# Kernel optimization log

Hardware: AMD Instinct MI355X
Metric: run time of the kernel (lower is better)

## Reference

```python
import jax, jax.numpy as jnp
import numpy as np

N, E = 50000, 800000
IN_F, HID, NCLS, NLAYERS = 64, 64, 2, 3
BN_EPS = 1e-5


def batch_norm(x, gamma, beta):
    # training-mode BatchNorm1d: biased batch statistics over the node/edge dim
    m = jnp.mean(x, axis=0)
    v = jnp.var(x, axis=0)
    return gamma * (x - m) * jax.lax.rsqrt(v + BN_EPS) + beta


def setup_inputs() -> dict:
    key = jax.random.key(0)
    ks = jax.random.split(key, 24)
    L, Lp1 = NLAYERS, NLAYERS + 1

    def lin(k, fan_in, shape):
        bound = 1.0 / np.sqrt(fan_in)
        return jax.random.uniform(k, shape, jnp.float32, -bound, bound)

    return {
        "h": jax.random.normal(ks[0], (N, IN_F), jnp.float32),
        "src": jax.random.randint(ks[1], (E,), 0, N, jnp.int32),
        "dst": jax.random.randint(ks[2], (E,), 0, N, jnp.int32),
        "emb_W": lin(ks[3], IN_F, (IN_F, HID)),
        "emb_b": lin(ks[4], IN_F, (HID,)),
        "mlp_W1": lin(ks[5], HID, (L, HID, HID)),
        "mlp_b1": lin(ks[6], HID, (L, HID)),
        "mlp_bn_g": jnp.ones((L, HID), jnp.float32),
        "mlp_bn_b": jnp.zeros((L, HID), jnp.float32),
        "mlp_W2": lin(ks[7], HID, (L, HID, HID)),
        "mlp_b2": lin(ks[8], HID, (L, HID)),
        "apply_bn_g": jnp.ones((L, HID), jnp.float32),
        "apply_bn_b": jnp.zeros((L, HID), jnp.float32),
        "out_bn_g": jnp.ones((L, HID), jnp.float32),
        "out_bn_b": jnp.zeros((L, HID), jnp.float32),
        "pred_W1": lin(ks[9], 2 * HID, (Lp1, 2 * HID, HID)),
        "pred_b1": lin(ks[10], 2 * HID, (Lp1, HID)),
        "pred_W2": lin(ks[11], HID, (Lp1, HID, NCLS)),
        "pred_b2": lin(ks[12], HID, (Lp1, NCLS)),
    }


def reference(h, src, dst, emb_W, emb_b, mlp_W1, mlp_b1, mlp_bn_g, mlp_bn_b,
              mlp_W2, mlp_b2, apply_bn_g, apply_bn_b, out_bn_g, out_bn_b,
              pred_W1, pred_b1, pred_W2, pred_b2):
    n_layers = mlp_W1.shape[0]
    n_nodes = h.shape[0]

    def edge_feat(hn):
        # concat src and dst node features per edge -> [E, 2*HID]
        return jnp.concatenate([hn[src], hn[dst]], axis=1)

    hn = h @ emb_W + emb_b  # embedding_h
    edge_reps = [edge_feat(hn)]

    for i in range(n_layers):
        # GINConv (sum aggregation, eps=0): (1+eps)*h_v + sum_{u->v} h_u
        agg = jax.ops.segment_sum(hn[src], dst, num_segments=n_nodes)
        z = hn + agg
        # MLP (depth 2): Linear -> BN -> ReLU -> Linear
        z = jax.nn.relu(batch_norm(z @ mlp_W1[i] + mlp_b1[i], mlp_bn_g[i], mlp_bn_b[i]))
        z = z @ mlp_W2[i] + mlp_b2[i]
        # ApplyNodeFunc: BN + ReLU
        z = jax.nn.relu(batch_norm(z, apply_bn_g[i], apply_bn_b[i]))
        # outer per-layer BN + ReLU
        hn = jax.nn.relu(batch_norm(z, out_bn_g[i], out_bn_b[i]))
        edge_reps.append(edge_feat(hn))

    # sum of per-layer edge predictions: Linear(2h->h) -> ReLU -> Linear(h->ncls)
    score = jnp.zeros((src.shape[0], pred_W2.shape[-1]), h.dtype)
    for i, e in enumerate(edge_reps):
        score = score + jax.nn.relu(e @ pred_W1[i] + pred_b1[i]) @ pred_W2[i] + pred_b2[i]
    return score
```

## Files before the change

### kernel.cpp

```cpp
#include <hip/hip_runtime.h>
#include <hip/hip_bf16.h>


#define BN_EPS 1e-5f

static __device__ __forceinline__ float bf2f(ushort u) {
  return __uint_as_float(((unsigned)u) << 16);
}

__global__ __launch_bounds__(256) void hist_kernel(const int* __restrict__ dst,
                                                   int* __restrict__ deg, int E) {
  int i = blockIdx.x * blockDim.x + threadIdx.x;
  int stride = gridDim.x * blockDim.x;
  for (; i < E; i += stride) atomicAdd(&deg[dst[i]], 1);
}

__global__ __launch_bounds__(256) void scan1_kernel(const int* __restrict__ deg,
                                                    int* __restrict__ rowstart,
                                                    int* __restrict__ partials, int N) {
  __shared__ int wsum[4];
  int tid = threadIdx.x;
  int lane = tid & 63, w = tid >> 6;
  int base = blockIdx.x * 1024 + tid * 4;
  int d0 = 0, d1 = 0, d2 = 0, d3 = 0;
  if (base + 3 < N) {
    int4 v = *reinterpret_cast<const int4*>(deg + base);
    d0 = v.x; d1 = v.y; d2 = v.z; d3 = v.w;
  } else {
    if (base + 0 < N) d0 = deg[base + 0];
    if (base + 1 < N) d1 = deg[base + 1];
    if (base + 2 < N) d2 = deg[base + 2];
  }
  int t0 = d0, t1 = t0 + d1, t2 = t1 + d2, t3 = t2 + d3;
  int tot = t3;
  int inc = tot;
#pragma unroll
  for (int off = 1; off < 64; off <<= 1) {
    int v = __shfl_up(inc, off);
    if (lane >= off) inc += v;
  }
  if (lane == 63) wsum[w] = inc;
  __syncthreads();
  int woff = 0;
  for (int k = 0; k < w; ++k) woff += wsum[k];
  int excl = woff + inc - tot;
  if (base + 0 < N) rowstart[base + 0] = excl;
  if (base + 1 < N) rowstart[base + 1] = excl + t0;
  if (base + 2 < N) rowstart[base + 2] = excl + t1;
  if (base + 3 < N) rowstart[base + 3] = excl + t2;
  if (tid == 255) partials[blockIdx.x] = excl + t3;
}

__global__ __launch_bounds__(64) void scan2_kernel(int* __restrict__ partials,
                                                   int* __restrict__ rowstart_end,
                                                   int NB) {
  int lane = threadIdx.x;
  int v = (lane < NB) ? partials[lane] : 0;
  int inc = v;
#pragma unroll
  for (int off = 1; off < 64; off <<= 1) {
    int t = __shfl_up(inc, off);
    if (lane >= off) inc += t;
  }
  if (lane < NB) partials[lane] = inc - v;
  if (lane == 63) *rowstart_end = inc;
}

__global__ __launch_bounds__(256) void scan3_kernel(const int* __restrict__ partials,
                                                    int* __restrict__ rowstart,
                                                    int* __restrict__ cursor, int N) {
  int off = partials[blockIdx.x];
  int base = blockIdx.x * 1024 + threadIdx.x * 4;
#pragma unroll
  for (int k = 0; k < 4; ++k) {
    int i = base + k;
    if (i < N) {
      int r = rowstart[i] + off;
      rowstart[i] = r;
      cursor[i] = r;
    }
  }
}

__global__ __launch_bounds__(256) void fill_kernel(const int* __restrict__ src,
                                                   const int* __restrict__ dst,
                                                   int* __restrict__ cursor,
                                                   int* __restrict__ eidx,
                                                   int* __restrict__ eord, int E) {
  int i = blockIdx.x * blockDim.x + threadIdx.x;
  int stride = gridDim.x * blockDim.x;
  for (; i < E; i += stride) {
    int p = atomicAdd(&cursor[dst[i]], 1);
    eidx[p] = src[i];
    eord[p] = i;
  }
}

template <int TR>
__global__ __launch_bounds__(256) void agg_kernel(
    const float* __restrict__ c, const ushort* __restrict__ cb,
    const int* __restrict__ rowstart, const int* __restrict__ eidx,
    const float* __restrict__ stats_in, const float* __restrict__ g_in,
    const float* __restrict__ b_in, float* __restrict__ z, int N) {
  int lane = threadIdx.x & 63;
  int v = blockIdx.x * 4 + (threadIdx.x >> 6);
  if (v >= N) return;
  float sc = 1.f, sh = 0.f;
  if (TR) {
    float invN = 1.0f / (float)N;
    float m = stats_in[lane] * invN;
    float var = stats_in[64 + lane] * invN - m * m;
    sc = g_in[lane] * rsqrtf(var + BN_EPS);
    sh = b_in[lane] - m * sc;
  }
  float x0 = c[(size_t)v * 64 + lane];
  float acc = TR ? fmaxf(x0 * sc + sh, 0.f) : x0;
  int p = rowstart[v], pe = rowstart[v + 1];
  for (; p + 8 <= pe; p += 8) {
    int u[8];
#pragma unroll
    for (int k = 0; k < 8; ++k) u[k] = eidx[p + k];
    float x[8];
#pragma unroll
    for (int k = 0; k < 8; ++k) x[k] = bf2f(cb[(size_t)u[k] * 64 + lane]);
#pragma unroll
    for (int k = 0; k < 8; ++k) acc += TR ? fmaxf(x[k] * sc + sh, 0.f) : x[k];
  }
  if (p + 4 <= pe) {
    int u[4];
#pragma unroll
    for (int k = 0; k < 4; ++k) u[k] = eidx[p + k];
#pragma unroll
    for (int k = 0; k < 4; ++k) {
      float x = bf2f(cb[(size_t)u[k] * 64 + lane]);
      acc += TR ? fmaxf(x * sc + sh, 0.f) : x;
    }
    p += 4;
  }
  for (; p < pe; ++p) {
    float x = bf2f(cb[(size_t)eidx[p] * 64 + lane]);
    acc += TR ? fmaxf(x * sc + sh, 0.f) : x;
  }
  z[(size_t)v * 64 + lane] = acc;
}

__global__ __launch_bounds__(256) void gemm64_kernel(
    const float* __restrict__ in, const float* __restrict__ W,
    const float* __restrict__ bias, const float* __restrict__ stats_in,
    const float* __restrict__ g_in, const float* __restrict__ b_in,
    float* __restrict__ out, float* __restrict__ stats_out,
    __hip_bfloat16* __restrict__ out_bf, int N) {
  __shared__ float sW[64][64];
  __shared__ float sx[32][64];
  __shared__ float red[2][4][64];
  int tid = threadIdx.x;
  int lane = tid & 63, w = tid >> 6;
  int n0 = blockIdx.x * 32;
#pragma unroll
  for (int r = 0; r < 16; ++r) {
    int idx = r * 256 + tid;
    sW[idx >> 6][idx & 63] = W[idx];
  }
  float sc = 1.f, sh = 0.f;
  if (stats_in) {
    float invN = 1.0f / (float)N;
    float m = stats_in[lane] * invN;
    float var = stats_in[64 + lane] * invN - m * m;
    sc = g_in[lane] * rsqrtf(var + BN_EPS);
    sh = b_in[lane] - m * sc;
  }
#pragma unroll
  for (int r = 0; r < 8; ++r) {
    int idx = r * 256 + tid;
    int n = n0 + (idx >> 6);
    float x = (n < N) ? in[(size_t)n * 64 + lane] : 0.f;
    if (stats_in) x = fmaxf(x * sc + sh, 0.f);
    sx[idx >> 6][lane] = x;
  }
  __syncthreads();
  float acc[8];
  float bz = bias ? bias[lane] : 0.f;
#pragma unroll
  for (int j = 0; j < 8; ++j) acc[j] = bz;
  for (int k = 0; k < 64; ++k) {
    float wv = sW[k][lane];
#pragma unroll
    for (int j = 0; j < 8; ++j) acc[j] = fmaf(sx[w * 8 + j][k], wv, acc[j]);
  }
  float ps = 0.f, pq = 0.f;
#pragma unroll
  for (int j = 0; j < 8; ++j) {
    int n = n0 + w * 8 + j;
    if (n < N) {
      out[(size_t)n * 64 + lane] = acc[j];
      if (out_bf) out_bf[(size_t)n * 64 + lane] = __float2bfloat16(acc[j]);
      ps += acc[j];
      pq += acc[j] * acc[j];
    }
  }
  if (stats_out) {
    red[0][w][lane] = ps;
    red[1][w][lane] = pq;
    __syncthreads();
    if (w == 0) {
      float s = red[0][0][lane] + red[0][1][lane] + red[0][2][lane] + red[0][3][lane];
      float q = red[1][0][lane] + red[1][1][lane] + red[1][2][lane] + red[1][3][lane];
      atomicAdd(&stats_out[lane], s);
      atomicAdd(&stats_out[64 + lane], q);
    }
  }
}

__global__ __launch_bounds__(256) void proj_kernel(
    const float* __restrict__ c, const float* __restrict__ W1,
    const float* __restrict__ b1, const float* __restrict__ stats_in,
    const float* __restrict__ g_in, const float* __restrict__ b_in,
    __hip_bfloat16* __restrict__ P1, __hip_bfloat16* __restrict__ P2, int N) {
  __shared__ float sWa[64][64];
  __shared__ float sWb[64][64];
  __shared__ float sx[32][64];
  int tid = threadIdx.x, lane = tid & 63, w = tid >> 6;
  int n0 = blockIdx.x * 32;
#pragma unroll
  for (int r = 0; r < 16; ++r) {
    int idx = r * 256 + tid;
    sWa[idx >> 6][idx & 63] = W1[idx];
    sWb[idx >> 6][idx & 63] = W1[4096 + idx];
  }
  float sc = 1.f, sh = 0.f;
  if (stats_in) {
    float invN = 1.0f / (float)N;
    float m = stats_in[lane] * invN;
    float var = stats_in[64 + lane] * invN - m * m;
    sc = g_in[lane] * rsqrtf(var + BN_EPS);
    sh = b_in[lane] - m * sc;
  }
#pragma unroll
  for (int r = 0; r < 8; ++r) {
    int idx = r * 256 + tid;
    int n = n0 + (idx >> 6);
    float x = (n < N) ? c[(size_t)n * 64 + lane] : 0.f;
    if (stats_in) x = fmaxf(x * sc + sh, 0.f);
    sx[idx >> 6][lane] = x;
  }
  __syncthreads();
  float a1[8], a2[8];
  float bz = b1[lane];
#pragma unroll
  for (int j = 0; j < 8; ++j) { a1[j] = bz; a2[j] = 0.f; }
  for (int k = 0; k < 64; ++k) {
    float wa = sWa[k][lane];
    float wb = sWb[k][lane];
#pragma unroll
    for (int j = 0; j < 8; ++j) {
      float x = sx[w * 8 + j][k];
      a1[j] = fmaf(x, wa, a1[j]);
      a2[j] = fmaf(x, wb, a2[j]);
    }
  }
#pragma unroll
  for (int j = 0; j < 8; ++j) {
    int n = n0 + w * 8 + j;
    if (n < N) {
      P1[(size_t)n * 64 + lane] = __float2bfloat16(a1[j]);
      P2[(size_t)n * 64 + lane] = __float2bfloat16(a2[j]);
    }
  }
}

__global__ __launch_bounds__(256) void bnrelu_kernel(
    const float* __restrict__ in, const float* __restrict__ stats_in,
    const float* __restrict__ g_in, const float* __restrict__ b_in,
    float* __restrict__ out, float* __restrict__ stats_out,
    __hip_bfloat16* __restrict__ out_bf, int N) {
  __shared__ float red[2][4][64];
  int tid = threadIdx.x;
  int lane = tid & 63, w = tid >> 6;
  float invN = 1.0f / (float)N;
  float m = stats_in[lane] * invN;
  float var = stats_in[64 + lane] * invN - m * m;
  float sc = g_in[lane] * rsqrtf(var + BN_EPS);
  float sh = b_in[lane] - m * sc;
  float ps = 0.f, pq = 0.f;
  int rows_per_grid = gridDim.x * (blockDim.x >> 6);
  for (int n = blockIdx.x * (blockDim.x >> 6) + w; n < N; n += rows_per_grid) {
    float x = fmaxf(in[(size_t)n * 64 + lane] * sc + sh, 0.f);
    out[(size_t)n * 64 + lane] = x;
    if (out_bf) out_bf[(size_t)n * 64 + lane] = __float2bfloat16(x);
    ps += x;
    pq += x * x;
  }
  if (stats_out) {
    red[0][w][lane] = ps;
    red[1][w][lane] = pq;
    __syncthreads();
    if (w == 0) {
      float s = red[0][0][lane] + red[0][1][lane] + red[0][2][lane] + red[0][3][lane];
      float q = red[1][0][lane] + red[1][1][lane] + red[1][2][lane] + red[1][3][lane];
      atomicAdd(&stats_out[lane], s);
      atomicAdd(&stats_out[64 + lane], q);
    }
  }
}

__global__ __launch_bounds__(256) void edge_score_csr_kernel(
    const ushort* __restrict__ P1, const ushort* __restrict__ P2,
    const int* __restrict__ rowstart, const int* __restrict__ eidx,
    const int* __restrict__ eord, const float* __restrict__ W2,
    const float* __restrict__ b2, float* __restrict__ out, int N, int first) {
  int lane = threadIdx.x & 63;
  int v = blockIdx.x * 4 + (threadIdx.x >> 6);
  if (v >= N) return;
  int sub = lane & 7;
  int grp = lane >> 3;
  float w[16];
  const float4* wp = reinterpret_cast<const float4*>(W2 + sub * 16);
#pragma unroll
  for (int k = 0; k < 4; ++k) {
    float4 t = wp[k];
    w[4 * k + 0] = t.x; w[4 * k + 1] = t.y; w[4 * k + 2] = t.z; w[4 * k + 3] = t.w;
  }
  float bb0 = b2[0], bb1 = b2[1];
  uint4 pb = *reinterpret_cast<const uint4*>(P2 + (size_t)v * 64 + sub * 8);
  unsigned bv[4] = {pb.x, pb.y, pb.z, pb.w};
  int p0 = rowstart[v], p1 = rowstart[v + 1];
  for (int p = p0 + grp; p < p1; p += 8) {
    int s = eidx[p];
    int e = eord[p];
    uint4 pa = *reinterpret_cast<const uint4*>(P1 + (size_t)s * 64 + sub * 8);
    unsigned av[4] = {pa.x, pa.y, pa.z, pa.w};
    float q0 = 0.f, q1 = 0.f;
#pragma unroll
    for (int k = 0; k < 4; ++k) {
      float a_lo = __uint_as_float(av[k] << 16);
      float a_hi = __uint_as_float(av[k] & 0xffff0000u);
      float b_lo = __uint_as_float(bv[k] << 16);
      float b_hi = __uint_as_float(bv[k] & 0xffff0000u);
      float v0 = fmaxf(a_lo + b_lo, 0.f);
      float v1 = fmaxf(a_hi + b_hi, 0.f);
      q0 = fmaf(v0, w[4 * k + 0], fmaf(v1, w[4 * k + 2], q0));
      q1 = fmaf(v0, w[4 * k + 1], fmaf(v1, w[4 * k + 3], q1));
    }
#pragma unroll
    for (int mm = 1; mm < 8; mm <<= 1) {
      q0 += __shfl_xor(q0, mm);
      q1 += __shfl_xor(q1, mm);
    }
    if (sub == 0) {
      float o0 = q0 + bb0, o1 = q1 + bb1;
      if (!first) {
        o0 += out[(size_t)e * 2];
        o1 += out[(size_t)e * 2 + 1];
      }
      out[(size_t)e * 2] = o0;
      out[(size_t)e * 2 + 1] = o1;
    }
  }
}

extern "C" void kernel_launch(void* const* d_in, const int* in_sizes, int n_in,
                              void* d_out, int out_size, void* d_ws, size_t ws_size,
                              hipStream_t stream) {
  const float* h          = (const float*)d_in[0];
  const int*   src        = (const int*)d_in[1];
  const int*   dst        = (const int*)d_in[2];
  const float* emb_W      = (const float*)d_in[3];
  const float* emb_b      = (const float*)d_in[4];
  const float* mlp_W1     = (const float*)d_in[5];
  const float* mlp_b1     = (const float*)d_in[6];
  const float* mlp_bn_g   = (const float*)d_in[7];
  const float* mlp_bn_b   = (const float*)d_in[8];
  const float* mlp_W2     = (const float*)d_in[9];
  const float* mlp_b2     = (const float*)d_in[10];
  const float* apply_bn_g = (const float*)d_in[11];
  const float* apply_bn_b = (const float*)d_in[12];
  const float* out_bn_g   = (const float*)d_in[13];
  const float* out_bn_b   = (const float*)d_in[14];
  const float* pred_W1    = (const float*)d_in[15];
  const float* pred_b1    = (const float*)d_in[16];
  const float* pred_W2    = (const float*)d_in[17];
  const float* pred_b2    = (const float*)d_in[18];

  const int N = in_sizes[0] / 64;
  const int E = in_sizes[1];
  const size_t NF = (size_t)N * 64;
  const int NB1 = (N + 1023) / 1024;

  float* ws = (float*)d_ws;
  float* c  = ws;
  float* zb = c + NF;
  float* z1 = zb + NF;
  float* z2 = z1 + NF;
  __hip_bfloat16* cb = (__hip_bfloat16*)(z2 + NF);
  __hip_bfloat16* P1 = cb + NF;
  __hip_bfloat16* P2 = P1 + NF;
  int* eidx     = (int*)(P2 + NF);
  int* eord     = eidx + E;
  int* rowstart = eord + E;
  int* cursor   = rowstart + (N + 64);
  int* partials = cursor + (N + 64);
  int* deg      = partials + 64;
  float* stats  = (float*)(deg + (N + 64));

  size_t need = (size_t)((char*)(stats + 9 * 128) - (char*)d_ws);
  if (need > ws_size) return;

  hipMemsetAsync(deg, 0, ((size_t)(N + 64) + 9 * 128) * sizeof(int), stream);

  const int gemmBlocks = (N + 31) / 32;
  const int nodeBlocks = (N + 3) / 4;

  gemm64_kernel<<<gemmBlocks, 256, 0, stream>>>(h, emb_W, emb_b, nullptr, nullptr,
                                                nullptr, c, nullptr, cb, N);
  hist_kernel<<<1024, 256, 0, stream>>>(dst, deg, E);
  scan1_kernel<<<NB1, 256, 0, stream>>>(deg, rowstart, partials, N);
  scan2_kernel<<<1, 64, 0, stream>>>(partials, rowstart + N, NB1);
  scan3_kernel<<<NB1, 256, 0, stream>>>(partials, rowstart, cursor, N);
  fill_kernel<<<1024, 256, 0, stream>>>(src, dst, cursor, eidx, eord, E);

  proj_kernel<<<gemmBlocks, 256, 0, stream>>>(c, pred_W1, pred_b1, nullptr, nullptr,
                                              nullptr, P1, P2, N);
  edge_score_csr_kernel<<<nodeBlocks, 256, 0, stream>>>(
      (const ushort*)P1, (const ushort*)P2, rowstart, eidx, eord, pred_W2, pred_b2,
      (float*)d_out, N, 1);

  for (int i = 0; i < 3; ++i) {
    float* st1 = stats + (size_t)(3 * i + 0) * 128;
    float* st2 = stats + (size_t)(3 * i + 1) * 128;
    float* st3 = stats + (size_t)(3 * i + 2) * 128;
    const float* stP = (i == 0) ? nullptr : stats + (size_t)(3 * (i - 1) + 2) * 128;
    const float* gP  = (i == 0) ? nullptr : out_bn_g + (i - 1) * 64;
    const float* bP  = (i == 0) ? nullptr : out_bn_b + (i - 1) * 64;

    if (i == 0)
      agg_kernel<0><<<nodeBlocks, 256, 0, stream>>>(c, (const ushort*)cb, rowstart,
                                                    eidx, nullptr, nullptr, nullptr,
                                                    zb, N);
    else
      agg_kernel<1><<<nodeBlocks, 256, 0, stream>>>(c, (const ushort*)cb, rowstart,
                                                    eidx, stP, gP, bP, zb, N);
    gemm64_kernel<<<gemmBlocks, 256, 0, stream>>>(zb, mlp_W1 + (size_t)i * 4096,
                                                  mlp_b1 + i * 64, nullptr, nullptr,
                                                  nullptr, z1, st1, nullptr, N);
    gemm64_kernel<<<gemmBlocks, 256, 0, stream>>>(z1, mlp_W2 + (size_t)i * 4096,
                                                  mlp_b2 + i * 64, st1,
                                                  mlp_bn_g + i * 64, mlp_bn_b + i * 64,
                                                  z2, st2, nullptr, N);
    bnrelu_kernel<<<784, 256, 0, stream>>>(z2, st2, apply_bn_g + i * 64,
                                           apply_bn_b + i * 64, c, st3, cb, N);
    proj_kernel<<<gemmBlocks, 256, 0, stream>>>(c, pred_W1 + (size_t)(i + 1) * 8192,
                                                pred_b1 + (i + 1) * 64, st3,
                                                out_bn_g + i * 64, out_bn_b + i * 64,
                                                P1, P2, N);
    edge_score_csr_kernel<<<nodeBlocks, 256, 0, stream>>>(
        (const ushort*)P1, (const ushort*)P2, rowstart, eidx, eord,
        pred_W2 + (i + 1) * 128, pred_b2 + (i + 1) * 2, (float*)d_out, N, 0);
  }
}
```

Before: 928.1 us.

## Fuse aggregation into first MLP GEMM, pack CSR edges, accumulate scores in CSR order

Fuses the GIN neighbour aggregation with the first MLP linear layer, so the aggregated features go straight into shared memory instead of a round trip through a global buffer. Packs the CSR source index and original edge id into one int2 array. Edge scores now accumulate in CSR order, coalesced, in a scratch buffer, with a single scatter at the end replacing the random read-modify-write per layer. The second scan kernel is folded into the third. The trade-off is that each fused block now gathers 8 nodes per wave serially, which cuts parallelism in the gather phase, and the extra scatter pass adds traffic.

```diff
diff --git a/kernel.cpp b/kernel.cpp
--- a/kernel.cpp
+++ b/kernel.cpp
@@ -51,26 +51,25 @@
   if (tid == 255) partials[blockIdx.x] = excl + t3;
 }
 
-__global__ __launch_bounds__(64) void scan2_kernel(int* __restrict__ partials,
-                                                   int* __restrict__ rowstart_end,
-                                                   int NB) {
-  int lane = threadIdx.x;
-  int v = (lane < NB) ? partials[lane] : 0;
-  int inc = v;
-#pragma unroll
-  for (int off = 1; off < 64; off <<= 1) {
-    int t = __shfl_up(inc, off);
-    if (lane >= off) inc += t;
-  }
-  if (lane < NB) partials[lane] = inc - v;
-  if (lane == 63) *rowstart_end = inc;
-}
-
 __global__ __launch_bounds__(256) void scan3_kernel(const int* __restrict__ partials,
                                                     int* __restrict__ rowstart,
-                                                    int* __restrict__ cursor, int N) {
-  int off = partials[blockIdx.x];
-  int base = blockIdx.x * 1024 + threadIdx.x * 4;
+                                                    int* __restrict__ cursor,
+                                                    int N, int NB, int E) {
+  __shared__ int s_off;
+  int tid = threadIdx.x;
+  if (tid < 64) {
+    int v = (tid < NB) ? partials[tid] : 0;
+    int inc = v;
+#pragma unroll
+    for (int off = 1; off < 64; off <<= 1) {
+      int t = __shfl_up(inc, off);
+      if (tid >= off) inc += t;
+    }
+    if (tid == (int)blockIdx.x) s_off = inc - v;
+  }
+  __syncthreads();
+  int off = s_off;
+  int base = blockIdx.x * 1024 + tid * 4;
 #pragma unroll
   for (int k = 0; k < 4; ++k) {
     int i = base + k;
@@ -80,68 +79,102 @@
       cursor[i] = r;
     }
   }
+  if (blockIdx.x == 0 && tid == 0) rowstart[N] = E;
 }
 
 __global__ __launch_bounds__(256) void fill_kernel(const int* __restrict__ src,
                                                    const int* __restrict__ dst,
                                                    int* __restrict__ cursor,
-                                                   int* __restrict__ eidx,
-                                                   int* __restrict__ eord, int E) {
+                                                   int2* __restrict__ epack, int E) {
   int i = blockIdx.x * blockDim.x + threadIdx.x;
   int stride = gridDim.x * blockDim.x;
   for (; i < E; i += stride) {
     int p = atomicAdd(&cursor[dst[i]], 1);
-    eidx[p] = src[i];
-    eord[p] = i;
+    epack[p] = make_int2(src[i], i);
   }
 }
 
 template <int TR>
-__global__ __launch_bounds__(256) void agg_kernel(
+__global__ __launch_bounds__(256) void agg_gemm_kernel(
     const float* __restrict__ c, const ushort* __restrict__ cb,
-    const int* __restrict__ rowstart, const int* __restrict__ eidx,
-    const float* __restrict__ stats_in, const float* __restrict__ g_in,
-    const float* __restrict__ b_in, float* __restrict__ z, int N) {
-  int lane = threadIdx.x & 63;
-  int v = blockIdx.x * 4 + (threadIdx.x >> 6);
-  if (v >= N) return;
+    const int2* __restrict__ epack, const int* __restrict__ rowstart,
+    const float* __restrict__ W, const float* __restrict__ bias,
+    const float* __restrict__ stats_tr, const float* __restrict__ g_tr,
+    const float* __restrict__ b_tr, float* __restrict__ out,
+    float* __restrict__ stats_out, int N) {
+  __shared__ float sW[64][64];
+  __shared__ float sx[32][64];
+  __shared__ float red[2][4][64];
+  int tid = threadIdx.x, lane = tid & 63, w = tid >> 6;
+  int n0 = blockIdx.x * 32;
+#pragma unroll
+  for (int r = 0; r < 16; ++r) {
+    int idx = r * 256 + tid;
+    sW[idx >> 6][idx & 63] = W[idx];
+  }
   float sc = 1.f, sh = 0.f;
   if (TR) {
     float invN = 1.0f / (float)N;
-    float m = stats_in[lane] * invN;
-    float var = stats_in[64 + lane] * invN - m * m;
-    sc = g_in[lane] * rsqrtf(var + BN_EPS);
-    sh = b_in[lane] - m * sc;
-  }
-  float x0 = c[(size_t)v * 64 + lane];
-  float acc = TR ? fmaxf(x0 * sc + sh, 0.f) : x0;
-  int p = rowstart[v], pe = rowstart[v + 1];
-  for (; p + 8 <= pe; p += 8) {
-    int u[8];
-#pragma unroll
-    for (int k = 0; k < 8; ++k) u[k] = eidx[p + k];
-    float x[8];
-#pragma unroll
-    for (int k = 0; k < 8; ++k) x[k] = bf2f(cb[(size_t)u[k] * 64 + lane]);
-#pragma unroll
-    for (int k = 0; k < 8; ++k) acc += TR ? fmaxf(x[k] * sc + sh, 0.f) : x[k];
-  }
-  if (p + 4 <= pe) {
-    int u[4];
-#pragma unroll
-    for (int k = 0; k < 4; ++k) u[k] = eidx[p + k];
-#pragma unroll
-    for (int k = 0; k < 4; ++k) {
-      float x = bf2f(cb[(size_t)u[k] * 64 + lane]);
-      acc += TR ? fmaxf(x * sc + sh, 0.f) : x;
-    }
-    p += 4;
-  }
-  for (; p < pe; ++p) {
-    float x = bf2f(cb[(size_t)eidx[p] * 64 + lane]);
-    acc += TR ? fmaxf(x * sc + sh, 0.f) : x;
-  }
-  z[(size_t)v * 64 + lane] = acc;
+    float m = stats_tr[lane] * invN;
+    float var = stats_tr[64 + lane] * invN - m * m;
+    sc = g_tr[lane] * rsqrtf(var + BN_EPS);
+    sh = b_tr[lane] - m * sc;
+  }
+  for (int j = 0; j < 8; ++j) {
+    int v = n0 + w * 8 + j;
+    float acc = 0.f;
+    if (v < N) {
+      float x0 = c[(size_t)v * 64 + lane];
+      acc = TR ? fmaxf(x0 * sc + sh, 0.f) : x0;
+      int p = rowstart[v], pe = rowstart[v + 1];
+      for (; p + 8 <= pe; p += 8) {
+        int u[8];
+#pragma unroll
+        for (int k = 0; k < 8; ++k) u[k] = epack[p + k].x;
+        float x[8];
+#pragma unroll
+        for (int k = 0; k < 8; ++k) x[k] = bf2f(cb[(size_t)u[k] * 64 + lane]);
+#pragma unroll
+        for (int k = 0; k < 8; ++k) acc += TR ? fmaxf(x[k] * sc + sh, 0.f) : x[k];
+      }
+      for (; p < pe; ++p) {
+        float x = bf2f(cb[(size_t)epack[p].x * 64 + lane]);
+        acc += TR ? fmaxf(x * sc + sh, 0.f) : x;
+      }
+    }
+    sx[w * 8 + j][lane] = acc;
+  }
+  __syncthreads();
+  float o[8];
+  float bz = bias[lane];
+#pragma unroll
+  for (int j = 0; j < 8; ++j) o[j] = bz;
+  for (int k = 0; k < 64; ++k) {
+    float wv = sW[k][lane];
+#pragma unroll
+    for (int j = 0; j < 8; ++j) o[j] = fmaf(sx[w * 8 + j][k], wv, o[j]);
+  }
+  float ps = 0.f, pq = 0.f;
+#pragma unroll
+  for (int j = 0; j < 8; ++j) {
+    int n = n0 + w * 8 + j;
+    if (n < N) {
+      out[(size_t)n * 64 + lane] = o[j];
+      ps += o[j];
+      pq += o[j] * o[j];
+    }
+  }
+  if (stats_out) {
+    red[0][w][lane] = ps;
+    red[1][w][lane] = pq;
+    __syncthreads();
+    if (w == 0) {
+      float s = red[0][0][lane] + red[0][1][lane] + red[0][2][lane] + red[0][3][lane];
+      float q = red[1][0][lane] + red[1][1][lane] + red[1][2][lane] + red[1][3][lane];
+      atomicAdd(&stats_out[lane], s);
+      atomicAdd(&stats_out[64 + lane], q);
+    }
+  }
 }
 
 __global__ __launch_bounds__(256) void gemm64_kernel(
@@ -305,9 +338,9 @@
 
 __global__ __launch_bounds__(256) void edge_score_csr_kernel(
     const ushort* __restrict__ P1, const ushort* __restrict__ P2,
-    const int* __restrict__ rowstart, const int* __restrict__ eidx,
-    const int* __restrict__ eord, const float* __restrict__ W2,
-    const float* __restrict__ b2, float* __restrict__ out, int N, int first) {
+    const int* __restrict__ rowstart, const int2* __restrict__ epack,
+    const float* __restrict__ W2, const float* __restrict__ b2,
+    float2* __restrict__ sc, int N, int first) {
   int lane = threadIdx.x & 63;
   int v = blockIdx.x * 4 + (threadIdx.x >> 6);
   if (v >= N) return;
@@ -325,8 +358,7 @@
   unsigned bv[4] = {pb.x, pb.y, pb.z, pb.w};
   int p0 = rowstart[v], p1 = rowstart[v + 1];
   for (int p = p0 + grp; p < p1; p += 8) {
-    int s = eidx[p];
-    int e = eord[p];
+    int s = epack[p].x;
     uint4 pa = *reinterpret_cast<const uint4*>(P1 + (size_t)s * 64 + sub * 8);
     unsigned av[4] = {pa.x, pa.y, pa.z, pa.w};
     float q0 = 0.f, q1 = 0.f;
@@ -349,13 +381,21 @@
     if (sub == 0) {
       float o0 = q0 + bb0, o1 = q1 + bb1;
       if (!first) {
-        o0 += out[(size_t)e * 2];
-        o1 += out[(size_t)e * 2 + 1];
+        float2 prev = sc[p];
+        o0 += prev.x;
+        o1 += prev.y;
       }
-      out[(size_t)e * 2] = o0;
-      out[(size_t)e * 2 + 1] = o1;
-    }
-  }
+      sc[p] = make_float2(o0, o1);
+    }
+  }
+}
+
+__global__ __launch_bounds__(256) void scatter_kernel(const float2* __restrict__ sc,
+                                                      const int2* __restrict__ epack,
+                                                      float2* __restrict__ out, int E) {
+  int i = blockIdx.x * blockDim.x + threadIdx.x;
+  int stride = gridDim.x * blockDim.x;
+  for (; i < E; i += stride) out[epack[i].y] = sc[i];
 }
 
 extern "C" void kernel_launch(void* const* d_in, const int* in_sizes, int n_in,
@@ -388,19 +428,18 @@
 
   float* ws = (float*)d_ws;
   float* c  = ws;
-  float* zb = c + NF;
-  float* z1 = zb + NF;
+  float* z1 = c + NF;
   float* z2 = z1 + NF;
   __hip_bfloat16* cb = (__hip_bfloat16*)(z2 + NF);
   __hip_bfloat16* P1 = cb + NF;
   __hip_bfloat16* P2 = P1 + NF;
-  int* eidx     = (int*)(P2 + NF);
-  int* eord     = eidx + E;
-  int* rowstart = eord + E;
-  int* cursor   = rowstart + (N + 64);
-  int* partials = cursor + (N + 64);
-  int* deg      = partials + 64;
-  float* stats  = (float*)(deg + (N + 64));
+  int2*   epack  = (int2*)(P2 + NF);
+  float2* scbuf  = (float2*)(epack + E);
+  int* rowstart  = (int*)(scbuf + E);
+  int* cursor    = rowstart + (N + 64);
+  int* partials  = cursor + (N + 64);
+  int* deg       = partials + 64;
+  float* stats   = (float*)(deg + (N + 64));
 
   size_t need = (size_t)((char*)(stats + 9 * 128) - (char*)d_ws);
   if (need > ws_size) return;
@@ -414,15 +453,14 @@
                                                 nullptr, c, nullptr, cb, N);
   hist_kernel<<<1024, 256, 0, stream>>>(dst, deg, E);
   scan1_kernel<<<NB1, 256, 0, stream>>>(deg, rowstart, partials, N);
-  scan2_kernel<<<1, 64, 0, stream>>>(partials, rowstart + N, NB1);
-  scan3_kernel<<<NB1, 256, 0, stream>>>(partials, rowstart, cursor, N);
-  fill_kernel<<<1024, 256, 0, stream>>>(src, dst, cursor, eidx, eord, E);
+  scan3_kernel<<<NB1, 256, 0, stream>>>(partials, rowstart, cursor, N, NB1, E);
+  fill_kernel<<<1024, 256, 0, stream>>>(src, dst, cursor, epack, E);
 
   proj_kernel<<<gemmBlocks, 256, 0, stream>>>(c, pred_W1, pred_b1, nullptr, nullptr,
                                               nullptr, P1, P2, N);
   edge_score_csr_kernel<<<nodeBlocks, 256, 0, stream>>>(
-      (const ushort*)P1, (const ushort*)P2, rowstart, eidx, eord, pred_W2, pred_b2,
-      (float*)d_out, N, 1);
+      (const ushort*)P1, (const ushort*)P2, rowstart, epack, pred_W2, pred_b2,
+      scbuf, N, 1);
 
   for (int i = 0; i < 3; ++i) {
     float* st1 = stats + (size_t)(3 * i + 0) * 128;
@@ -433,15 +471,13 @@
     const float* bP  = (i == 0) ? nullptr : out_bn_b + (i - 1) * 64;
 
     if (i == 0)
-      agg_kernel<0><<<nodeBlocks, 256, 0, stream>>>(c, (const ushort*)cb, rowstart,
-                                                    eidx, nullptr, nullptr, nullptr,
-                                                    zb, N);
+      agg_gemm_kernel<0><<<gemmBlocks, 256, 0, stream>>>(
+          c, (const ushort*)cb, epack, rowstart, mlp_W1 + (size_t)i * 4096,
+          mlp_b1 + i * 64, nullptr, nullptr, nullptr, z1, st1, N);
     else
-      agg_kernel<1><<<nodeBlocks, 256, 0, stream>>>(c, (const ushort*)cb, rowstart,
-                                                    eidx, stP, gP, bP, zb, N);
-    gemm64_kernel<<<gemmBlocks, 256, 0, stream>>>(zb, mlp_W1 + (size_t)i * 4096,
-                                                  mlp_b1 + i * 64, nullptr, nullptr,
-                                                  nullptr, z1, st1, nullptr, N);
+      agg_gemm_kernel<1><<<gemmBlocks, 256, 0, stream>>>(
+          c, (const ushort*)cb, epack, rowstart, mlp_W1 + (size_t)i * 4096,
+          mlp_b1 + i * 64, stP, gP, bP, z1, st1, N);
     gemm64_kernel<<<gemmBlocks, 256, 0, stream>>>(z1, mlp_W2 + (size_t)i * 4096,
                                                   mlp_b2 + i * 64, st1,
                                                   mlp_bn_g + i * 64, mlp_bn_b + i * 64,
@@ -453,7 +489,9 @@
                                                 out_bn_g + i * 64, out_bn_b + i * 64,
                                                 P1, P2, N);
     edge_score_csr_kernel<<<nodeBlocks, 256, 0, stream>>>(
-        (const ushort*)P1, (const ushort*)P2, rowstart, eidx, eord,
-        pred_W2 + (i + 1) * 128, pred_b2 + (i + 1) * 2, (float*)d_out, N, 0);
-  }
-}
+        (const ushort*)P1, (const ushort*)P2, rowstart, epack,
+        pred_W2 + (i + 1) * 128, pred_b2 + (i + 1) * 2, scbuf, N, 0);
+  }
+
+  scatter_kernel<<<2048, 256, 0, stream>>>(scbuf, epack, (float2*)d_out, E);
+}
```

New measurement: 972.8 us. 4.8% more time.
